# Kernel tuning notes

Measured on AMD Instinct MI355X. Metric: run time of the kernel, lower is better.

## Reference

```python
import jax, jax.numpy as jnp
import numpy as np

N_NODES = 100000
N_EDGES = 320000
DIM = 128
BN_EPS = 1e-5
AGG_EPS = 1e-6


def setup_inputs() -> dict:
    key = jax.random.key(0)
    ks = jax.random.split(key, 12)
    s = 1.0 / np.sqrt(DIM)
    inp = {
        "x": jax.random.normal(ks[0], (N_NODES, DIM), dtype=jnp.float32),
        "e": jax.random.normal(ks[1], (N_EDGES, DIM), dtype=jnp.float32),
        "edge_index": jax.random.randint(ks[2], (2, N_EDGES), 0, N_NODES, dtype=jnp.int32),
        "Wa": jax.random.normal(ks[3], (DIM, DIM), dtype=jnp.float32) * s,
        "ba": jnp.zeros((DIM,), dtype=jnp.float32),
        "Wb": jax.random.normal(ks[4], (DIM, DIM), dtype=jnp.float32) * s,
        "bb": jnp.zeros((DIM,), dtype=jnp.float32),
        "Wd": jax.random.normal(ks[5], (DIM, DIM), dtype=jnp.float32) * s,
        "bd": jnp.zeros((DIM,), dtype=jnp.float32),
        "We": jax.random.normal(ks[6], (DIM, DIM), dtype=jnp.float32) * s,
        "be": jnp.zeros((DIM,), dtype=jnp.float32),
        "gamma": jnp.ones((DIM,), dtype=jnp.float32),
        "beta": jnp.zeros((DIM,), dtype=jnp.float32),
    }
    return inp


def reference(x, e, edge_index, Wa, ba, Wb, bb, Wd, bd, We, be, gamma, beta):
    # PyG source_to_target flow: j = edge_index[0] (source), i = edge_index[1] (target)
    src = edge_index[0]
    dst = edge_index[1]

    Ax = x @ Wa + ba
    Bx = x @ Wb + bb
    Dx = x @ Wd + bd
    Ex = x @ We + be

    # message: e_ij = Dx_i + Ex_j ; sigma = sigmoid(e_ij)  [n_edges, out_dim]
    e_ij = Dx[dst] + Ex[src]
    sigma = jax.nn.sigmoid(e_ij)

    # aggregate: gated mean over incoming edges of each target node
    num = jax.ops.segment_sum(sigma * Bx[src], dst, num_segments=N_NODES)
    den = jax.ops.segment_sum(sigma, dst, num_segments=N_NODES)
    aggr = num / (den + AGG_EPS)

    # update + BatchNorm (training stats, biased var) + ReLU; dropout=0, residual=False
    h = Ax + aggr
    mean = jnp.mean(h, axis=0)
    var = jnp.mean(jnp.square(h - mean), axis=0)
    h_norm = (h - mean) * jax.lax.rsqrt(var + BN_EPS)
    x_out = jax.nn.relu(gamma * h_norm + beta)

    # edge output is raw e_ij (bn_edge_e is never applied in forward)
    return x_out, e_ij
```

## Files before the change

### kernel.cpp

```cpp
#include <hip/hip_runtime.h>
#include <hip/hip_bf16.h>
#include <stdint.h>

#define N_NODES 100000
#define N_EDGES 320000
#define DIM 128
#define AGG_EPS 1e-6f
#define BN_EPS 1e-5f
#define NODE_BLOCKS 2048
#define SCAN_BLOCKS 391
#define GEMM_BLOCKS 782
#define EDGE_BLOCKS 1250

typedef float f32x4 __attribute__((ext_vector_type(4)));
typedef float f32x2 __attribute__((ext_vector_type(2)));
typedef __bf16 bf16x8 __attribute__((ext_vector_type(8)));

__device__ __forceinline__ uint32_t f2bf(float f) {
  union { float f; uint32_t u; } v; v.f = f;
  uint32_t u = v.u;
  return (u + 0x7fffu + ((u >> 16) & 1u)) >> 16;
}
__device__ __forceinline__ float bf2f(uint32_t h) {
  union { uint32_t u; float f; } v; v.u = h << 16;
  return v.f;
}
__device__ __forceinline__ void nt_store2(float* p, float a, float b) {
  f32x2 v = {a, b};
  __builtin_nontemporal_store(v, (f32x2*)p);
}


__global__ __launch_bounds__(256) void k_prep(
    const float* __restrict__ Wa, const float* __restrict__ ba,
    const float* __restrict__ Wb, const float* __restrict__ bb,
    const float* __restrict__ Wd, const float* __restrict__ bd,
    const float* __restrict__ We, const float* __restrict__ be,
    ushort* __restrict__ wt, float* __restrict__ biasc,
    uint4* __restrict__ cnt_zero, int* __restrict__ done) {
  __shared__ float tile[64][65];
  const int tid = threadIdx.x;
  const int b = blockIdx.x;
  const int sel = b >> 2, tr = (b >> 1) & 1, tc = b & 1;
  const float* W = (sel == 0) ? Wa : (sel == 1) ? Wb : (sel == 2) ? Wd : We;
#pragma unroll
  for (int i = 0; i < 16; ++i) {
    int idx = tid + 256 * i;
    int lr = idx >> 6, lc = idx & 63;
    tile[lr][lc] = W[(tr * 64 + lr) * 128 + tc * 64 + lc];
  }
  __syncthreads();
#pragma unroll
  for (int i = 0; i < 16; ++i) {
    int idx = tid + 256 * i;
    int oc = idx >> 6, ok = idx & 63;
    wt[(sel * 128 + tc * 64 + oc) * 128 + tr * 64 + ok] = (ushort)f2bf(tile[ok][oc]);
  }
  if (b == 0) {
    for (int t = tid; t < 512; t += 256) {
      int s2 = t >> 7;
      const float* bp = (s2 == 0) ? ba : (s2 == 1) ? bb : (s2 == 2) ? bd : be;
      biasc[t] = bp[t & 127];
    }
    if (tid == 0) *done = 0;
  }
  for (int j = b * 256 + tid; j < 25000; j += 16 * 256)
    cnt_zero[j] = make_uint4(0u, 0u, 0u, 0u);
}

__global__ __launch_bounds__(256) void k_gemm_count(
    const float* __restrict__ x, const ushort* __restrict__ wt,
    const float* __restrict__ biasc, ushort* __restrict__ abde,
    const int* __restrict__ dst, int* __restrict__ cnt) {
  __shared__ ushort As[128 * 128];
  __shared__ ushort Bs[64 * 128];
  const int tid = threadIdx.x;
  const int bid = blockIdx.x;

  if (bid >= GEMM_BLOCKS) {
    int e = (bid - GEMM_BLOCKS) * 256 + tid;
    if (e < N_EDGES) atomicAdd(&cnt[dst[e]], 1);
    return;
  }
  const int m0 = bid * 128;

#pragma unroll
  for (int i = 0; i < 8; ++i) {
    int qid = tid + 256 * i;
    int row = qid >> 4, q = qid & 15;
    int gr = m0 + row;
    uint4 pk = make_uint4(0u, 0u, 0u, 0u);
    if (gr < N_NODES) {
      const float* s = x + (size_t)gr * 128 + q * 8;
      float4 f0 = *(const float4*)(s);
      float4 f1 = *(const float4*)(s + 4);
      pk.x = f2bf(f0.x) | (f2bf(f0.y) << 16);
      pk.y = f2bf(f0.z) | (f2bf(f0.w) << 16);
      pk.z = f2bf(f1.x) | (f2bf(f1.y) << 16);
      pk.w = f2bf(f1.z) | (f2bf(f1.w) << 16);
    }
    int byte = (row * 256 + q * 16) ^ ((row & 7) << 4);
    *(uint4*)((char*)As + byte) = pk;
  }
  __syncthreads();

  const int w = tid >> 6, lane = tid & 63;
  const int r = lane & 15, g = lane >> 4;

  bf16x8 afrag[2][4];
#pragma unroll
  for (int m = 0; m < 2; ++m)
#pragma unroll
    for (int kk = 0; kk < 4; ++kk) {
      int arow = w * 32 + m * 16 + r;
      int ab = (arow * 256 + kk * 64 + g * 16) ^ ((arow & 7) << 4);
      afrag[m][kk] = *(const bf16x8*)((const char*)As + ab);
    }

  const int ntpair[4][2] = {{2, 6}, {3, 7}, {0, 4}, {1, 5}};
  for (int ph = 0; ph < 4; ++ph) {
    f32x4 acc[2][2][4] = {};
#pragma unroll
    for (int t2 = 0; t2 < 2; ++t2) {
      if (ph | t2) __syncthreads();
      const int n0 = ntpair[ph][t2] * 64;
#pragma unroll
      for (int i = 0; i < 4; ++i) {
        int qid = tid + 256 * i;
        int row = qid >> 4, q = qid & 15;
        uint4 v = *(const uint4*)(wt + (n0 + row) * 128 + q * 8);
        int byte = (row * 256 + q * 16) ^ ((row & 7) << 4);
        *(uint4*)((char*)Bs + byte) = v;
      }
      __syncthreads();
#pragma unroll
      for (int kk = 0; kk < 4; ++kk) {
        bf16x8 bv[4];
#pragma unroll
        for (int n = 0; n < 4; ++n) {
          int brow = n * 16 + r;
          int bb = (brow * 256 + kk * 64 + g * 16) ^ ((brow & 7) << 4);
          bv[n] = *(const bf16x8*)((const char*)Bs + bb);
        }
#pragma unroll
        for (int m = 0; m < 2; ++m)
#pragma unroll
          for (int n = 0; n < 4; ++n)
            acc[t2][m][n] = __builtin_amdgcn_mfma_f32_16x16x32_bf16(
                afrag[m][kk], bv[n], acc[t2][m][n], 0, 0, 0);
      }
    }
#pragma unroll
    for (int t2 = 0; t2 < 2; ++t2) {
#pragma unroll
      for (int m = 0; m < 2; ++m) {
#pragma unroll
        for (int n = 0; n < 4; ++n) {
          int lc = t2 * 64 + n * 16 + r;
          float bsv = biasc[ntpair[ph][t2] * 64 + n * 16 + r];
#pragma unroll
          for (int q = 0; q < 4; ++q) {
            int row = w * 32 + m * 16 + g * 4 + q;
            As[row * 128 + (lc ^ (((row >> 2) & 3) << 4))] =
                (ushort)f2bf(acc[t2][m][n][q] + bsv);
          }
        }
      }
    }
    __syncthreads();
#pragma unroll
    for (int it = 0; it < 8; ++it) {
      int u = tid + 256 * it;
      int row = u >> 4, mq = u & 15;
      int xo = ((row >> 2) & 3) << 4;
      uint2 lo = *(const uint2*)&As[row * 128 + ((4 * mq) ^ xo)];
      uint2 hi = *(const uint2*)&As[row * 128 + ((64 + 4 * mq) ^ xo)];
      uint4 val = (ph < 2) ? make_uint4(hi.x, lo.x, hi.y, lo.y)
                           : make_uint4(lo.x, hi.x, lo.y, hi.y);
      int gr = m0 + row;
      if (gr < N_NODES)
        *(uint4*)((char*)abde + (size_t)gr * 1024 + (ph * 16 + mq) * 16) = val;
    }
  }
}

__global__ __launch_bounds__(256) void k_bsum(const int* __restrict__ cnt,
                                              int* __restrict__ bsum2) {
  __shared__ int lds[256];
  int t = threadIdx.x;
  int i = blockIdx.x * 256 + t;
  lds[t] = (i < N_NODES) ? cnt[i] : 0;
  __syncthreads();
#pragma unroll
  for (int off = 128; off > 0; off >>= 1) {
    if (t < off) lds[t] += lds[t + off];
    __syncthreads();
  }
  if (t == 0) bsum2[blockIdx.x] = lds[0];
}

__global__ __launch_bounds__(256) void k_scan(const int* __restrict__ cnt,
                                              const int* __restrict__ bsum2,
                                              int* __restrict__ row_ptr,
                                              int* __restrict__ cursor) {
  __shared__ int ps[256];
  __shared__ int lds[256];
  __shared__ int boff_s;
  const int t = threadIdx.x;
  int a = (2 * t < SCAN_BLOCKS) ? bsum2[2 * t] : 0;
  int b = (2 * t + 1 < SCAN_BLOCKS) ? bsum2[2 * t + 1] : 0;
  ps[t] = a + b;
  __syncthreads();
  for (int off = 1; off < 256; off <<= 1) {
    int v = (t >= off) ? ps[t - off] : 0;
    __syncthreads();
    ps[t] += v;
    __syncthreads();
  }
  if (t == 0) {
    int b0 = blockIdx.x, p = b0 >> 1;
    int pre = (p > 0) ? ps[p - 1] : 0;
    if (b0 & 1) pre += bsum2[b0 - 1];
    boff_s = pre;
  }
  int i = blockIdx.x * 256 + t;
  int v = (i < N_NODES) ? cnt[i] : 0;
  lds[t] = v;
  __syncthreads();
  for (int off = 1; off < 256; off <<= 1) {
    int u = (t >= off) ? lds[t - off] : 0;
    __syncthreads();
    lds[t] += u;
    __syncthreads();
  }
  if (i < N_NODES) {
    int ex = boff_s + lds[t] - v;
    row_ptr[i] = ex;
    cursor[i] = ex;
  }
  if (blockIdx.x == 0 && t == 0) row_ptr[N_NODES] = N_EDGES;
}

__global__ __launch_bounds__(256) void k_scatter(const int* __restrict__ dst,
                                                 const int* __restrict__ srcArr,
                                                 int* __restrict__ cursor,
                                                 int* __restrict__ csr_eid,
                                                 int* __restrict__ csr_src) {
  int t = blockIdx.x * 256 + threadIdx.x;
  if (t < N_EDGES) {
    int d = dst[t];
    int s = srcArr[t];
    int pos = atomicAdd(&cursor[d], 1);
    csr_eid[pos] = t;
    csr_src[pos] = s;
  }
}

__global__ __launch_bounds__(256) void k_node(
    const ushort* __restrict__ abde, const int* __restrict__ row_ptr,
    const int* __restrict__ csr_eid, const int* __restrict__ csr_src,
    float* __restrict__ out_e, ushort* __restrict__ h,
    float* __restrict__ partials) {
  const int tid = threadIdx.x;
  const int lane = tid & 63;
  const int wid = (blockIdx.x << 2) | (tid >> 6);
  const int nw = NODE_BLOCKS * 4;
  float s0 = 0.f, s1 = 0.f, q0 = 0.f, q1 = 0.f;

  int i = wid;
  int k0 = 0, ke = 0;
  uint2 ad = make_uint2(0u, 0u);
  if (i < N_NODES) {
    k0 = row_ptr[i];
    ke = row_ptr[i + 1];
    ad = *(const uint2*)((const char*)abde + (size_t)i * 1024 + 512 + lane * 8);
  }
  while (i < N_NODES) {
    const int inext = i + nw;
    int nk0 = 0, nke = 0;
    uint2 nad = make_uint2(0u, 0u);
    if (inext < N_NODES) {
      nk0 = row_ptr[inext];
      nke = row_ptr[inext + 1];
      nad = *(const uint2*)((const char*)abde + (size_t)inext * 1024 + 512 + lane * 8);
    }
    float ax0 = bf2f(ad.x & 0xffffu), ax1 = bf2f(ad.x >> 16);
    float dx0 = bf2f(ad.y & 0xffffu), dx1 = bf2f(ad.y >> 16);
    float n0 = 0.f, n1 = 0.f, d0 = 0.f, d1 = 0.f;
    for (int base = k0; base < ke; base += 64) {
      const int cnt = min(64, ke - base);
      int eidv = 0, srcv = 0;
      if (lane < cnt) {
        eidv = csr_eid[base + lane];
        srcv = csr_src[base + lane];
      }
      int j = 0;
      for (; j + 2 <= cnt; j += 2) {
        int eA = __shfl(eidv, j),     sA = __shfl(srcv, j);
        int eB = __shfl(eidv, j + 1), sB = __shfl(srcv, j + 1);
        uint2 ebA = *(const uint2*)((const char*)abde + (size_t)sA * 1024 + lane * 8);
        uint2 ebB = *(const uint2*)((const char*)abde + (size_t)sB * 1024 + lane * 8);
        float e0 = dx0 + bf2f(ebA.x & 0xffffu);
        float e1 = dx1 + bf2f(ebA.x >> 16);
        nt_store2(out_e + (size_t)eA * 128 + 2 * lane, e0, e1);
        float sg0 = 1.f / (1.f + __expf(-e0));
        float sg1 = 1.f / (1.f + __expf(-e1));
        n0 += sg0 * bf2f(ebA.y & 0xffffu); n1 += sg1 * bf2f(ebA.y >> 16);
        d0 += sg0; d1 += sg1;
        float f0 = dx0 + bf2f(ebB.x & 0xffffu);
        float f1 = dx1 + bf2f(ebB.x >> 16);
        nt_store2(out_e + (size_t)eB * 128 + 2 * lane, f0, f1);
        float tg0 = 1.f / (1.f + __expf(-f0));
        float tg1 = 1.f / (1.f + __expf(-f1));
        n0 += tg0 * bf2f(ebB.y & 0xffffu); n1 += tg1 * bf2f(ebB.y >> 16);
        d0 += tg0; d1 += tg1;
      }
      if (j < cnt) {
        int eA = __shfl(eidv, j), sA = __shfl(srcv, j);
        uint2 ebA = *(const uint2*)((const char*)abde + (size_t)sA * 1024 + lane * 8);
        float e0 = dx0 + bf2f(ebA.x & 0xffffu);
        float e1 = dx1 + bf2f(ebA.x >> 16);
        nt_store2(out_e + (size_t)eA * 128 + 2 * lane, e0, e1);
        float sg0 = 1.f / (1.f + __expf(-e0));
        float sg1 = 1.f / (1.f + __expf(-e1));
        n0 += sg0 * bf2f(ebA.y & 0xffffu); n1 += sg1 * bf2f(ebA.y >> 16);
        d0 += sg0; d1 += sg1;
      }
    }
    float h0 = ax0 + n0 / (d0 + AGG_EPS);
    float h1 = ax1 + n1 / (d1 + AGG_EPS);
    *(uint32_t*)(h + (size_t)i * 128 + 2 * lane) = f2bf(h0) | (f2bf(h1) << 16);
    s0 += h0; s1 += h1; q0 += h0 * h0; q1 += h1 * h1;
    i = inext; k0 = nk0; ke = nke; ad = nad;
  }
  __shared__ float red[256 * 4];
  red[tid] = s0; red[256 + tid] = s1; red[512 + tid] = q0; red[768 + tid] = q1;
  __syncthreads();
  if (tid < 64) {
    float vs0 = red[tid] + red[tid + 64] + red[tid + 128] + red[tid + 192];
    float vs1 = red[256 + tid] + red[256 + tid + 64] + red[256 + tid + 128] + red[256 + tid + 192];
    float vq0 = red[512 + tid] + red[512 + tid + 64] + red[512 + tid + 128] + red[512 + tid + 192];
    float vq1 = red[768 + tid] + red[768 + tid + 64] + red[768 + tid + 128] + red[768 + tid + 192];
    float* p = partials + blockIdx.x * 256;
    p[2 * tid] = vs0;
    p[2 * tid + 1] = vs1;
    p[128 + 2 * tid] = vq0;
    p[128 + 2 * tid + 1] = vq1;
  }
}

__global__ __launch_bounds__(256) void k_stats(const float* __restrict__ partials,
                                               float* __restrict__ out2,
                                               float* __restrict__ stats,
                                               int* __restrict__ done) {
  const int t = threadIdx.x, b = blockIdx.x;
  float s = 0.f;
#pragma unroll
  for (int j = 0; j < 32; ++j) s += partials[(b * 32 + j) * 256 + t];
  out2[b * 256 + t] = s;
  __threadfence();
  __shared__ int ticket;
  if (t == 0) ticket = atomicAdd(done, 1);
  __syncthreads();
  if (ticket == 63 && t < 128) {
    float ss = 0.f, qq = 0.f;
#pragma unroll
    for (int bb = 0; bb < 64; ++bb) {
      ss += out2[bb * 256 + t];
      qq += out2[bb * 256 + 128 + t];
    }
    float mean = ss * (1.f / (float)N_NODES);
    float var = qq * (1.f / (float)N_NODES) - mean * mean;
    stats[t] = mean;
    stats[128 + t] = rsqrtf(var + BN_EPS);
  }
}

__global__ __launch_bounds__(256) void k_final(const ushort* __restrict__ h,
    const float* __restrict__ gamma, const float* __restrict__ beta,
    const float* __restrict__ stats, float* __restrict__ out_x) {
  int idx = blockIdx.x * 256 + threadIdx.x;
  int c = (idx & 15) * 8;
  uint4 hv = *(const uint4*)(h + idx * 8);
  uint32_t hw[4] = {hv.x, hv.y, hv.z, hv.w};
  float out[8];
#pragma unroll
  for (int j = 0; j < 8; ++j) {
    uint32_t u = (j & 1) ? (hw[j >> 1] >> 16) : (hw[j >> 1] & 0xffffu);
    float hf = bf2f(u);
    int cc = c + j;
    float v = gamma[cc] * (hf - stats[cc]) * stats[128 + cc] + beta[cc];
    out[j] = fmaxf(v, 0.f);
  }
  f32x4 v0 = {out[0], out[1], out[2], out[3]};
  f32x4 v1 = {out[4], out[5], out[6], out[7]};
  __builtin_nontemporal_store(v0, (f32x4*)(out_x + idx * 8));
  __builtin_nontemporal_store(v1, (f32x4*)(out_x + idx * 8 + 4));
}

extern "C" void kernel_launch(void* const* d_in, const int* in_sizes, int n_in,
                              void* d_out, int out_size, void* d_ws, size_t ws_size,
                              hipStream_t stream) {
  const float* x = (const float*)d_in[0];
  const int* edge_index = (const int*)d_in[2];
  const float* Wa = (const float*)d_in[3];
  const float* ba = (const float*)d_in[4];
  const float* Wb = (const float*)d_in[5];
  const float* bb = (const float*)d_in[6];
  const float* Wd = (const float*)d_in[7];
  const float* bd = (const float*)d_in[8];
  const float* We = (const float*)d_in[9];
  const float* be = (const float*)d_in[10];
  const float* gamma = (const float*)d_in[11];
  const float* beta = (const float*)d_in[12];

  const int* src = edge_index;
  const int* dst = edge_index + N_EDGES;

  char* w = (char*)d_ws;
  ushort* wt      = (ushort*)(w);
  float*  biasc   = (float*)(w + 131072);
  ushort* abde    = (ushort*)(w + 133120);
  ushort* hbuf    = (ushort*)(w + 102533120);
  int*    cnt     = (int*)(w + 128133120);
  int*    row_ptr = (int*)(w + 128533120);
  int*    cursor  = (int*)(w + 128933248);
  int*    csr_eid = (int*)(w + 129333248);
  float*  partials= (float*)(w + 130613248);
  float*  stats   = (float*)(w + 132710400);

  int*   bsum2 = (int*)partials;
  float* out2  = (float*)cnt;
  int*   done  = row_ptr + 100001;

  float* out_x = (float*)d_out;
  float* out_e = out_x + (size_t)N_NODES * DIM;
  int* csr_src = (int*)out_x;

  k_prep<<<16, 256, 0, stream>>>(Wa, ba, Wb, bb, Wd, bd, We, be, wt, biasc,
                                 (uint4*)cnt, done);
  k_gemm_count<<<GEMM_BLOCKS + EDGE_BLOCKS, 256, 0, stream>>>(x, wt, biasc, abde, dst, cnt);
  k_bsum<<<SCAN_BLOCKS, 256, 0, stream>>>(cnt, bsum2);
  k_scan<<<SCAN_BLOCKS, 256, 0, stream>>>(cnt, bsum2, row_ptr, cursor);
  k_scatter<<<EDGE_BLOCKS, 256, 0, stream>>>(dst, src, cursor, csr_eid, csr_src);
  k_node<<<NODE_BLOCKS, 256, 0, stream>>>(abde, row_ptr, csr_eid, csr_src, out_e, hbuf, partials);
  k_stats<<<64, 256, 0, stream>>>(partials, out2, stats, done);
  k_final<<<6250, 256, 0, stream>>>(hbuf, gamma, beta, stats, out_x);
}
```

Baseline: 168.6 us.

## Split edge-output write into separate edge-ordered kernel, drop CSR edge-id array

Moves the e_ij output write out of the CSR node loop into a new kernel that walks edges in their original order, so out_e stores become sequential rather than scattered by edge id. This lets the scatter step and the node kernel drop the csr_eid array. The cost is a second gather of Dx[dst] and Ex[src] per edge and one more kernel launch. csr_src also moves from the output buffer into the workspace slot that csr_eid used.

```diff
diff --git a/kernel.cpp b/kernel.cpp
--- a/kernel.cpp
+++ b/kernel.cpp
@@ -184,6 +184,31 @@
   }
 }
 
+__global__ __launch_bounds__(256) void k_edge(
+    const int* __restrict__ dst, const int* __restrict__ srcArr,
+    const ushort* __restrict__ abde, float* __restrict__ out_e) {
+  const int lane = threadIdx.x & 63;
+  const int wid = (blockIdx.x << 2) | (threadIdx.x >> 6);
+  const int base = wid * 64;
+  const int dv = dst[base + lane];
+  const int sv = srcArr[base + lane];
+#pragma unroll 2
+  for (int j = 0; j < 64; j += 2) {
+    int dA = __shfl(dv, j),     sA = __shfl(sv, j);
+    int dB = __shfl(dv, j + 1), sB = __shfl(sv, j + 1);
+    uint2 adA = *(const uint2*)((const char*)abde + (size_t)dA * 1024 + 512 + lane * 8);
+    uint2 ebA = *(const uint2*)((const char*)abde + (size_t)sA * 1024 + lane * 8);
+    uint2 adB = *(const uint2*)((const char*)abde + (size_t)dB * 1024 + 512 + lane * 8);
+    uint2 ebB = *(const uint2*)((const char*)abde + (size_t)sB * 1024 + lane * 8);
+    float e0 = bf2f(adA.y & 0xffffu) + bf2f(ebA.x & 0xffffu);
+    float e1 = bf2f(adA.y >> 16) + bf2f(ebA.x >> 16);
+    nt_store2(out_e + (size_t)(base + j) * 128 + 2 * lane, e0, e1);
+    float f0 = bf2f(adB.y & 0xffffu) + bf2f(ebB.x & 0xffffu);
+    float f1 = bf2f(adB.y >> 16) + bf2f(ebB.x >> 16);
+    nt_store2(out_e + (size_t)(base + j + 1) * 128 + 2 * lane, f0, f1);
+  }
+}
+
 __global__ __launch_bounds__(256) void k_bsum(const int* __restrict__ cnt,
                                               int* __restrict__ bsum2) {
   __shared__ int lds[256];
@@ -244,23 +269,20 @@
 __global__ __launch_bounds__(256) void k_scatter(const int* __restrict__ dst,
                                                  const int* __restrict__ srcArr,
                                                  int* __restrict__ cursor,
-                                                 int* __restrict__ csr_eid,
                                                  int* __restrict__ csr_src) {
   int t = blockIdx.x * 256 + threadIdx.x;
   if (t < N_EDGES) {
     int d = dst[t];
     int s = srcArr[t];
     int pos = atomicAdd(&cursor[d], 1);
-    csr_eid[pos] = t;
     csr_src[pos] = s;
   }
 }
 
 __global__ __launch_bounds__(256) void k_node(
     const ushort* __restrict__ abde, const int* __restrict__ row_ptr,
-    const int* __restrict__ csr_eid, const int* __restrict__ csr_src,
-    float* __restrict__ out_e, ushort* __restrict__ h,
-    float* __restrict__ partials) {
+    const int* __restrict__ csr_src,
+    ushort* __restrict__ h, float* __restrict__ partials) {
   const int tid = threadIdx.x;
   const int lane = tid & 63;
   const int wid = (blockIdx.x << 2) | (tid >> 6);
@@ -289,38 +311,32 @@
     float n0 = 0.f, n1 = 0.f, d0 = 0.f, d1 = 0.f;
     for (int base = k0; base < ke; base += 64) {
       const int cnt = min(64, ke - base);
-      int eidv = 0, srcv = 0;
-      if (lane < cnt) {
-        eidv = csr_eid[base + lane];
-        srcv = csr_src[base + lane];
-      }
+      int srcv = 0;
+      if (lane < cnt) srcv = csr_src[base + lane];
       int j = 0;
       for (; j + 2 <= cnt; j += 2) {
-        int eA = __shfl(eidv, j),     sA = __shfl(srcv, j);
-        int eB = __shfl(eidv, j + 1), sB = __shfl(srcv, j + 1);
+        int sA = __shfl(srcv, j);
+        int sB = __shfl(srcv, j + 1);
         uint2 ebA = *(const uint2*)((const char*)abde + (size_t)sA * 1024 + lane * 8);
         uint2 ebB = *(const uint2*)((const char*)abde + (size_t)sB * 1024 + lane * 8);
         float e0 = dx0 + bf2f(ebA.x & 0xffffu);
         float e1 = dx1 + bf2f(ebA.x >> 16);
-        nt_store2(out_e + (size_t)eA * 128 + 2 * lane, e0, e1);
         float sg0 = 1.f / (1.f + __expf(-e0));
         float sg1 = 1.f / (1.f + __expf(-e1));
         n0 += sg0 * bf2f(ebA.y & 0xffffu); n1 += sg1 * bf2f(ebA.y >> 16);
         d0 += sg0; d1 += sg1;
         float f0 = dx0 + bf2f(ebB.x & 0xffffu);
         float f1 = dx1 + bf2f(ebB.x >> 16);
-        nt_store2(out_e + (size_t)eB * 128 + 2 * lane, f0, f1);
         float tg0 = 1.f / (1.f + __expf(-f0));
         float tg1 = 1.f / (1.f + __expf(-f1));
         n0 += tg0 * bf2f(ebB.y & 0xffffu); n1 += tg1 * bf2f(ebB.y >> 16);
         d0 += tg0; d1 += tg1;
       }
       if (j < cnt) {
-        int eA = __shfl(eidv, j), sA = __shfl(srcv, j);
+        int sA = __shfl(srcv, j);
         uint2 ebA = *(const uint2*)((const char*)abde + (size_t)sA * 1024 + lane * 8);
         float e0 = dx0 + bf2f(ebA.x & 0xffffu);
         float e1 = dx1 + bf2f(ebA.x >> 16);
-        nt_store2(out_e + (size_t)eA * 128 + 2 * lane, e0, e1);
         float sg0 = 1.f / (1.f + __expf(-e0));
         float sg1 = 1.f / (1.f + __expf(-e1));
         n0 += sg0 * bf2f(ebA.y & 0xffffu); n1 += sg1 * bf2f(ebA.y >> 16);
@@ -425,7 +441,7 @@
   int*    cnt     = (int*)(w + 128133120);
   int*    row_ptr = (int*)(w + 128533120);
   int*    cursor  = (int*)(w + 128933248);
-  int*    csr_eid = (int*)(w + 129333248);
+  int*    csr_src = (int*)(w + 129333248);
   float*  partials= (float*)(w + 130613248);
   float*  stats   = (float*)(w + 132710400);
 
@@ -435,15 +451,15 @@
 
   float* out_x = (float*)d_out;
   float* out_e = out_x + (size_t)N_NODES * DIM;
-  int* csr_src = (int*)out_x;
 
   k_prep<<<16, 256, 0, stream>>>(Wa, ba, Wb, bb, Wd, bd, We, be, wt, biasc,
                                  (uint4*)cnt, done);
   k_gemm_count<<<GEMM_BLOCKS + EDGE_BLOCKS, 256, 0, stream>>>(x, wt, biasc, abde, dst, cnt);
+  k_edge<<<1250, 256, 0, stream>>>(dst, src, abde, out_e);
   k_bsum<<<SCAN_BLOCKS, 256, 0, stream>>>(cnt, bsum2);
   k_scan<<<SCAN_BLOCKS, 256, 0, stream>>>(cnt, bsum2, row_ptr, cursor);
-  k_scatter<<<EDGE_BLOCKS, 256, 0, stream>>>(dst, src, cursor, csr_eid, csr_src);
-  k_node<<<NODE_BLOCKS, 256, 0, stream>>>(abde, row_ptr, csr_eid, csr_src, out_e, hbuf, partials);
+  k_scatter<<<EDGE_BLOCKS, 256, 0, stream>>>(dst, src, cursor, csr_src);
+  k_node<<<NODE_BLOCKS, 256, 0, stream>>>(abde, row_ptr, csr_src, hbuf, partials);
   k_stats<<<64, 256, 0, stream>>>(partials, out2, stats, done);
   k_final<<<6250, 256, 0, stream>>>(hbuf, gamma, beta, stats, out_x);
 }
```

Result: slower. 215.5 us (+27.8%).
